# Performance work log

Hardware: AMD Instinct MI355X
Metric: run time of the kernel (lower is better)

The kernel has to match this reference:

```python
import jax, jax.numpy as jnp
import numpy as np

# lower-triangular <-> 3x3 symmetric matrix index maps (match torch_lotri2mat/mat2lotri)
LOTRI = np.array([[0, 1, 3], [1, 2, 4], [3, 4, 5]])
ROWS = np.array([0, 1, 1, 2, 2, 2])
COLS = np.array([0, 0, 1, 0, 1, 2])
NUM_NEWTON_ITERS = 6


def det3(A):
    # A: (N,3,3)
    return (A[:, 0, 0] * (A[:, 1, 1] * A[:, 2, 2] - A[:, 1, 2] * A[:, 2, 1])
            - A[:, 0, 1] * (A[:, 1, 0] * A[:, 2, 2] - A[:, 1, 2] * A[:, 2, 0])
            + A[:, 0, 2] * (A[:, 1, 0] * A[:, 2, 1] - A[:, 1, 1] * A[:, 2, 0]))


def inv3(A):
    # closed-form 3x3 inverse via adjugate; A: (N,3,3)
    c00 = A[:, 1, 1] * A[:, 2, 2] - A[:, 1, 2] * A[:, 2, 1]
    c01 = A[:, 0, 2] * A[:, 2, 1] - A[:, 0, 1] * A[:, 2, 2]
    c02 = A[:, 0, 1] * A[:, 1, 2] - A[:, 0, 2] * A[:, 1, 1]
    c10 = A[:, 1, 2] * A[:, 2, 0] - A[:, 1, 0] * A[:, 2, 2]
    c11 = A[:, 0, 0] * A[:, 2, 2] - A[:, 0, 2] * A[:, 2, 0]
    c12 = A[:, 0, 2] * A[:, 1, 0] - A[:, 0, 0] * A[:, 1, 2]
    c20 = A[:, 1, 0] * A[:, 2, 1] - A[:, 1, 1] * A[:, 2, 0]
    c21 = A[:, 0, 1] * A[:, 2, 0] - A[:, 0, 0] * A[:, 2, 1]
    c22 = A[:, 0, 0] * A[:, 1, 1] - A[:, 0, 1] * A[:, 1, 0]
    adj = jnp.stack([jnp.stack([c00, c01, c02], -1),
                     jnp.stack([c10, c11, c12], -1),
                     jnp.stack([c20, c21, c22], -1)], -2)  # (N,3,3)
    det = (A[:, 0, 0] * c00 + A[:, 0, 1] * c10 + A[:, 0, 2] * c20)
    return adj / det[:, None, None]


def trilinear_warp(img, ddf):
    # img: (B,C,H,W,D), ddf: (B,3,H,W,D) in voxel units; border padding (clamped corners)
    B, C, H, W, D = img.shape
    base = jnp.stack(jnp.meshgrid(jnp.arange(H), jnp.arange(W), jnp.arange(D),
                                  indexing='ij'), 0).astype(img.dtype)  # (3,H,W,D)
    coords = base[None] + ddf                                           # (B,3,H,W,D)
    c0 = jnp.floor(coords)
    frac = coords - c0
    c0i = c0.astype(jnp.int32)
    dims = jnp.array([H, W, D], jnp.int32).reshape(1, 3, 1, 1, 1)
    lo = jnp.clip(c0i, 0, dims - 1)
    hi = jnp.clip(c0i + 1, 0, dims - 1)
    imgf = img.reshape(B, C, H * W * D)

    def gather(xi, yi, zi):
        lin = (xi * W + yi) * D + zi                      # (B,H,W,D)
        idx = jnp.broadcast_to(lin.reshape(B, 1, -1), (B, C, H * W * D))
        return jnp.take_along_axis(imgf, idx, axis=2).reshape(B, C, H, W, D)

    fx, fy, fz = frac[:, 0, None], frac[:, 1, None], frac[:, 2, None]  # (B,1,H,W,D)
    x0, y0, z0 = lo[:, 0], lo[:, 1], lo[:, 2]
    x1, y1, z1 = hi[:, 0], hi[:, 1], hi[:, 2]
    out = jnp.zeros_like(img)
    for xi, wx in ((x0, 1.0 - fx), (x1, fx)):
        for yi, wy in ((y0, 1.0 - fy), (y1, fy)):
            for zi, wz in ((z0, 1.0 - fz), (z1, fz)):
                out = out + wx * wy * wz * gather(xi, yi, zi)
    return out


def ddf_jacobian(ddf):
    # Jacobian of the deformation phi(x)=x+ddf(x): J = I + d(ddf_i)/dx_j (central differences)
    rows = []
    for i in range(3):
        g = jnp.gradient(ddf[:, i], axis=(1, 2, 3))  # list of 3 arrays (B,H,W,D)
        rows.append(jnp.stack(g, axis=1))
    J = jnp.stack(rows, axis=1)                      # (B,3,3,H,W,D)
    eye = jnp.eye(3, dtype=ddf.dtype).reshape(1, 3, 3, 1, 1, 1)
    return J + eye


def newton_polar_det(X, n_iters):
    # Newton iteration for polar decomposition with determinant scaling
    U = X
    for _ in range(n_iters):
        zeta = jnp.abs(det3(U)) ** (-1.0 / 3.0)
        zU = zeta[:, None, None] * U
        U = 0.5 * (zU + inv3(jnp.swapaxes(zU, -1, -2)))
    return U


def setup_inputs() -> dict:
    key = jax.random.key(0)
    k1, k2 = jax.random.split(key)
    B, H, W, D = 2, 128, 128, 128
    dti = jax.random.normal(k1, (B, 6, H, W, D), dtype=jnp.float32)
    # smooth, realistic displacement field so J = I + grad(ddf) is well-conditioned
    g = jnp.stack(jnp.meshgrid(jnp.arange(H), jnp.arange(W), jnp.arange(D),
                               indexing='ij'), 0).astype(jnp.float32) / H  # (3,H,W,D)
    two_pi = 2.0 * jnp.pi
    amp = 2.0
    ddf = amp * jnp.stack([jnp.sin(two_pi * (g[0] + 0.5 * g[1])),
                           jnp.cos(two_pi * (g[1] + 0.5 * g[2])),
                           jnp.sin(two_pi * (g[2] + 0.5 * g[0]))], 0)  # (3,H,W,D)
    ddf = jnp.broadcast_to(ddf[None], (B, 3, H, W, D))
    ddf = ddf + 0.02 * jax.random.normal(k2, (B, 3, H, W, D), dtype=jnp.float32)
    return {"dti": dti, "ddf": ddf}


def reference(dti, ddf):
    B, _, H, W, D = dti.shape
    # 1) warp the lower-triangular DTI with trilinear interpolation (border padding)
    warped_lotri = trilinear_warp(dti, ddf)              # (B,6,H,W,D)
    # 2) lotri -> 3x3 symmetric matrices, absorb spatial dims
    Dmat = warped_lotri[:, LOTRI]                        # (B,3,3,H,W,D)
    Dns = Dmat.transpose(0, 3, 4, 5, 1, 2).reshape(-1, 3, 3)
    # 3) Jacobian of DDF, absorb spatial dims
    J = ddf_jacobian(ddf)                                # (B,3,3,H,W,D)
    Jns = J.transpose(0, 3, 4, 5, 1, 2).reshape(-1, 3, 3)
    # 4) rotation from polar decomposition (Newton, det scaling)
    R = newton_polar_det(Jns, NUM_NEWTON_ITERS)          # (N,3,3)
    # 5) finite-strain reorientation: R^T D R per voxel
    out_ns = jnp.einsum('nji,njk,nkl->nil', R, Dns, R)
    # 6) expand spatial dims, mat -> lotri
    out_mat = out_ns.reshape(B, H, W, D, 3, 3).transpose(0, 4, 5, 1, 2, 3)
    return out_mat[:, ROWS, COLS]                        # (B,6,H,W,D)
```

## Files before the change

### kernel.cpp

```cpp
#include <hip/hip_runtime.h>

#define NH 128
#define NW 128
#define ND 128
#define HWD (NH * NW * ND)
#define NWD (NW * ND)
#define NB 2

__global__ __launch_bounds__(256) void warp_dti_kernel(
    const float* __restrict__ dti,
    const float* __restrict__ ddf,
    float* __restrict__ out)
{
    const int blk   = blockIdx.x;
    const int b     = blk >> 13;
    const int blkin = blk & 8191;
    const int tid   = threadIdx.x;
    const int sp    = (blkin << 8) | tid;
    const int d     = tid & (ND - 1);
    const int w     = ((blkin & 63) << 1) | (tid >> 7);
    const int h     = blkin >> 6;

    const int dbase = b * 3 * HWD;

    const int oh_m = (h > 0)      ? -NWD : 0;
    const int oh_p = (h < NH - 1) ?  NWD : 0;
    const int ow_m = (w > 0)      ? -ND  : 0;
    const int ow_p = (w < NW - 1) ?  ND  : 0;
    const int od_m = (d > 0)      ? -1   : 0;
    const int od_p = (d < ND - 1) ?  1   : 0;

    float uc[3], hm[3], hp[3], wm[3], wp[3], dm[3], dp[3];
#pragma unroll
    for (int c = 0; c < 3; ++c) {
        const float* p = ddf + dbase + c * HWD;
        uc[c] = p[sp];
    }
#pragma unroll
    for (int c = 0; c < 3; ++c) {
        const float* p = ddf + dbase + c * HWD;
        hm[c] = p[sp + oh_m];  hp[c] = p[sp + oh_p];
        wm[c] = p[sp + ow_m];  wp[c] = p[sp + ow_p];
        dm[c] = p[sp + od_m];  dp[c] = p[sp + od_p];
    }

    const float cx = (float)h + uc[0];
    const float cy = (float)w + uc[1];
    const float cz = (float)d + uc[2];
    const float flx = floorf(cx), fly = floorf(cy), flz = floorf(cz);
    const float fx = cx - flx, fy = cy - fly, fz = cz - flz;
    const int x0 = (int)flx, y0 = (int)fly, z0 = (int)flz;
    const int xa = min(max(x0,     0), NH - 1), xb = min(max(x0 + 1, 0), NH - 1);
    const int ya = min(max(y0,     0), NW - 1), yb = min(max(y0 + 1, 0), NW - 1);
    const int za = min(max(z0,     0), ND - 1), zb = min(max(z0 + 1, 0), ND - 1);

    const int raa = (xa * NW + ya) * ND;
    const int rab = (xa * NW + yb) * ND;
    const int rba = (xb * NW + ya) * ND;
    const int rbb = (xb * NW + yb) * ND;

    int lin[8];
    lin[0] = raa + za; lin[1] = raa + zb;
    lin[2] = rab + za; lin[3] = rab + zb;
    lin[4] = rba + za; lin[5] = rba + zb;
    lin[6] = rbb + za; lin[7] = rbb + zb;

    const int ibase = b * 6 * HWD;
    float g[8][6];
#pragma unroll
    for (int c = 0; c < 8; ++c)
#pragma unroll
        for (int ch = 0; ch < 6; ++ch)
            g[c][ch] = dti[ibase + ch * HWD + lin[c]];

    __builtin_amdgcn_sched_barrier(0);

    const float sh = (oh_m == 0 || oh_p == 0) ? 1.0f : 0.5f;
    const float sw = (ow_m == 0 || ow_p == 0) ? 1.0f : 0.5f;
    const float sd = (od_m == 0 || od_p == 0) ? 1.0f : 0.5f;

    float U[3][3];
#pragma unroll
    for (int c = 0; c < 3; ++c) {
        U[c][0] = sh * (hp[c] - hm[c]);
        U[c][1] = sw * (wp[c] - wm[c]);
        U[c][2] = sd * (dp[c] - dm[c]);
    }
    U[0][0] += 1.0f; U[1][1] += 1.0f; U[2][2] += 1.0f;

#pragma unroll
    for (int it = 0; it < 6; ++it) {
        float c00 = U[1][1]*U[2][2] - U[1][2]*U[2][1];
        float c01 = U[0][2]*U[2][1] - U[0][1]*U[2][2];
        float c02 = U[0][1]*U[1][2] - U[0][2]*U[1][1];
        float c10 = U[1][2]*U[2][0] - U[1][0]*U[2][2];
        float c11 = U[0][0]*U[2][2] - U[0][2]*U[2][0];
        float c12 = U[0][2]*U[1][0] - U[0][0]*U[1][2];
        float c20 = U[1][0]*U[2][1] - U[1][1]*U[2][0];
        float c21 = U[0][1]*U[2][0] - U[0][0]*U[2][1];
        float c22 = U[0][0]*U[1][1] - U[0][1]*U[1][0];
        float det = U[0][0]*c00 + U[0][1]*c10 + U[0][2]*c20;

        float l    = __log2f(fabsf(det));
        float zeta = __builtin_amdgcn_exp2f(-0.33333333333333333f * l);
        float s    = copysignf(zeta * zeta, det);
        float hz = 0.5f * zeta;
        float hs = 0.5f * s;

        float n00 = hz*U[0][0] + c00*hs;
        float n01 = hz*U[0][1] + c10*hs;
        float n02 = hz*U[0][2] + c20*hs;
        float n10 = hz*U[1][0] + c01*hs;
        float n11 = hz*U[1][1] + c11*hs;
        float n12 = hz*U[1][2] + c21*hs;
        float n20 = hz*U[2][0] + c02*hs;
        float n21 = hz*U[2][1] + c12*hs;
        float n22 = hz*U[2][2] + c22*hs;
        U[0][0]=n00; U[0][1]=n01; U[0][2]=n02;
        U[1][0]=n10; U[1][1]=n11; U[1][2]=n12;
        U[2][0]=n20; U[2][1]=n21; U[2][2]=n22;
    }

    const float wxa = 1.0f - fx, wya = 1.0f - fy, wza = 1.0f - fz;
    float wc[8];
    wc[0] = (wxa * wya) * wza;  wc[1] = (wxa * wya) * fz;
    wc[2] = (wxa * fy)  * wza;  wc[3] = (wxa * fy)  * fz;
    wc[4] = (fx  * wya) * wza;  wc[5] = (fx  * wya) * fz;
    wc[6] = (fx  * fy)  * wza;  wc[7] = (fx  * fy)  * fz;

    float acc[6] = {0.f, 0.f, 0.f, 0.f, 0.f, 0.f};
#pragma unroll
    for (int c = 0; c < 8; ++c)
#pragma unroll
        for (int ch = 0; ch < 6; ++ch)
            acc[ch] = fmaf(wc[c], g[c][ch], acc[ch]);

    float Dm[3][3];
    Dm[0][0] = acc[0]; Dm[0][1] = acc[1]; Dm[0][2] = acc[3];
    Dm[1][0] = acc[1]; Dm[1][1] = acc[2]; Dm[1][2] = acc[4];
    Dm[2][0] = acc[3]; Dm[2][1] = acc[4]; Dm[2][2] = acc[5];

    float M[3][3];
#pragma unroll
    for (int i = 0; i < 3; ++i)
#pragma unroll
        for (int k = 0; k < 3; ++k)
            M[i][k] = U[0][i]*Dm[0][k] + U[1][i]*Dm[1][k] + U[2][i]*Dm[2][k];

    float T00 = M[0][0]*U[0][0] + M[0][1]*U[1][0] + M[0][2]*U[2][0];
    float T10 = M[1][0]*U[0][0] + M[1][1]*U[1][0] + M[1][2]*U[2][0];
    float T11 = M[1][0]*U[0][1] + M[1][1]*U[1][1] + M[1][2]*U[2][1];
    float T20 = M[2][0]*U[0][0] + M[2][1]*U[1][0] + M[2][2]*U[2][0];
    float T21 = M[2][0]*U[0][1] + M[2][1]*U[1][1] + M[2][2]*U[2][1];
    float T22 = M[2][0]*U[0][2] + M[2][1]*U[1][2] + M[2][2]*U[2][2];

    const int obase = b * 6 * HWD;
    out[obase + 0 * HWD + sp] = T00;
    out[obase + 1 * HWD + sp] = T10;
    out[obase + 2 * HWD + sp] = T11;
    out[obase + 3 * HWD + sp] = T20;
    out[obase + 4 * HWD + sp] = T21;
    out[obase + 5 * HWD + sp] = T22;
}

extern "C" void kernel_launch(void* const* d_in, const int* in_sizes, int n_in,
                              void* d_out, int out_size, void* d_ws, size_t ws_size,
                              hipStream_t stream) {
    const float* dti = (const float*)d_in[0];
    const float* ddf = (const float*)d_in[1];
    float* o = (float*)d_out;
    const int n = NB * HWD;
    warp_dti_kernel<<<n / 256, 256, 0, stream>>>(dti, ddf, o);
}
```

Before: 299.3 us.

## Pair z-neighbor gathers into dwordx2 loads and overlap them with Newton iterations

The 48 scalar gathers of the trilinear warp become 24 64-bit loads, each fetching both z-neighbours. Clamping the z index to ND-2 keeps the pair in range, and the weights are remapped so border clamping still gives the same result. The loads are issued through inline asm before the Newton polar iterations, with an explicit vmcnt wait placed after them, so the gather latency overlaps the ALU work. The risks are the unaligned 8-byte accesses, the fragility of hand-written asm (raw waitcnt, sgpr base constraint), and higher register pressure from keeping loads in flight.

```diff
diff --git a/kernel.cpp b/kernel.cpp
--- a/kernel.cpp
+++ b/kernel.cpp
@@ -6,6 +6,8 @@
 #define HWD (NH * NW * ND)
 #define NWD (NW * ND)
 #define NB 2
+
+typedef float f32x2 __attribute__((ext_vector_type(2)));
 
 __global__ __launch_bounds__(256) void warp_dti_kernel(
     const float* __restrict__ dti,
@@ -35,45 +37,10 @@
     for (int c = 0; c < 3; ++c) {
         const float* p = ddf + dbase + c * HWD;
         uc[c] = p[sp];
-    }
-#pragma unroll
-    for (int c = 0; c < 3; ++c) {
-        const float* p = ddf + dbase + c * HWD;
         hm[c] = p[sp + oh_m];  hp[c] = p[sp + oh_p];
         wm[c] = p[sp + ow_m];  wp[c] = p[sp + ow_p];
         dm[c] = p[sp + od_m];  dp[c] = p[sp + od_p];
     }
-
-    const float cx = (float)h + uc[0];
-    const float cy = (float)w + uc[1];
-    const float cz = (float)d + uc[2];
-    const float flx = floorf(cx), fly = floorf(cy), flz = floorf(cz);
-    const float fx = cx - flx, fy = cy - fly, fz = cz - flz;
-    const int x0 = (int)flx, y0 = (int)fly, z0 = (int)flz;
-    const int xa = min(max(x0,     0), NH - 1), xb = min(max(x0 + 1, 0), NH - 1);
-    const int ya = min(max(y0,     0), NW - 1), yb = min(max(y0 + 1, 0), NW - 1);
-    const int za = min(max(z0,     0), ND - 1), zb = min(max(z0 + 1, 0), ND - 1);
-
-    const int raa = (xa * NW + ya) * ND;
-    const int rab = (xa * NW + yb) * ND;
-    const int rba = (xb * NW + ya) * ND;
-    const int rbb = (xb * NW + yb) * ND;
-
-    int lin[8];
-    lin[0] = raa + za; lin[1] = raa + zb;
-    lin[2] = rab + za; lin[3] = rab + zb;
-    lin[4] = rba + za; lin[5] = rba + zb;
-    lin[6] = rbb + za; lin[7] = rbb + zb;
-
-    const int ibase = b * 6 * HWD;
-    float g[8][6];
-#pragma unroll
-    for (int c = 0; c < 8; ++c)
-#pragma unroll
-        for (int ch = 0; ch < 6; ++ch)
-            g[c][ch] = dti[ibase + ch * HWD + lin[c]];
-
-    __builtin_amdgcn_sched_barrier(0);
 
     const float sh = (oh_m == 0 || oh_p == 0) ? 1.0f : 0.5f;
     const float sw = (ow_m == 0 || ow_p == 0) ? 1.0f : 0.5f;
@@ -87,6 +54,37 @@
         U[c][2] = sd * (dp[c] - dm[c]);
     }
     U[0][0] += 1.0f; U[1][1] += 1.0f; U[2][2] += 1.0f;
+
+    const float cx = (float)h + uc[0];
+    const float cy = (float)w + uc[1];
+    const float cz = (float)d + uc[2];
+    const float flx = floorf(cx), fly = floorf(cy), flz = floorf(cz);
+    const float fx = cx - flx, fy = cy - fly, fz = cz - flz;
+    const int x0 = (int)flx, y0 = (int)fly, z0 = (int)flz;
+    const int xa = min(max(x0,     0), NH - 1), xb = min(max(x0 + 1, 0), NH - 1);
+    const int ya = min(max(y0,     0), NW - 1), yb = min(max(y0 + 1, 0), NW - 1);
+    const int pa = min(max(z0, 0), ND - 2);
+
+    unsigned voffs[4];
+    voffs[0] = (unsigned)(((xa * NW + ya) * ND) + pa) * 4u;
+    voffs[1] = (unsigned)(((xa * NW + yb) * ND) + pa) * 4u;
+    voffs[2] = (unsigned)(((xb * NW + ya) * ND) + pa) * 4u;
+    voffs[3] = (unsigned)(((xb * NW + yb) * ND) + pa) * 4u;
+
+    const float* bases[6];
+#pragma unroll
+    for (int ch = 0; ch < 6; ++ch)
+        bases[ch] = dti + (size_t)(b * 6 + ch) * HWD;
+
+    __builtin_amdgcn_sched_barrier(0);
+    f32x2 g[6][4];
+#pragma unroll
+    for (int ch = 0; ch < 6; ++ch)
+#pragma unroll
+        for (int c = 0; c < 4; ++c)
+            asm volatile("global_load_dwordx2 %0, %1, %2"
+                         : "=v"(g[ch][c])
+                         : "v"(voffs[c]), "s"(bases[ch]));
 
 #pragma unroll
     for (int it = 0; it < 6; ++it) {
@@ -121,19 +119,26 @@
         U[2][0]=n20; U[2][1]=n21; U[2][2]=n22;
     }
 
-    const float wxa = 1.0f - fx, wya = 1.0f - fy, wza = 1.0f - fz;
-    float wc[8];
-    wc[0] = (wxa * wya) * wza;  wc[1] = (wxa * wya) * fz;
-    wc[2] = (wxa * fy)  * wza;  wc[3] = (wxa * fy)  * fz;
-    wc[4] = (fx  * wya) * wza;  wc[5] = (fx  * wya) * fz;
-    wc[6] = (fx  * fy)  * wza;  wc[7] = (fx  * fy)  * fz;
+    const float wza = 1.0f - fz, wzb = fz;
+    const float wv0 = ((z0 <= ND - 2) ? wza : 0.0f) + ((z0 <= -1) ? wzb : 0.0f);
+    const float wv1 = ((z0 >= ND - 1) ? wza : 0.0f) + ((z0 >=  0) ? wzb : 0.0f);
+    const float wxa = 1.0f - fx, wya = 1.0f - fy;
+    float wxy[4];
+    wxy[0] = wxa * wya;  wxy[1] = wxa * fy;
+    wxy[2] = fx  * wya;  wxy[3] = fx  * fy;
+    float wA[4], wB[4];
+#pragma unroll
+    for (int c = 0; c < 4; ++c) { wA[c] = wxy[c] * wv0; wB[c] = wxy[c] * wv1; }
+
+    asm volatile("s_waitcnt vmcnt(0)" ::: "memory");
+    __builtin_amdgcn_sched_barrier(0);
 
     float acc[6] = {0.f, 0.f, 0.f, 0.f, 0.f, 0.f};
 #pragma unroll
-    for (int c = 0; c < 8; ++c)
+    for (int c = 0; c < 4; ++c)
 #pragma unroll
         for (int ch = 0; ch < 6; ++ch)
-            acc[ch] = fmaf(wc[c], g[c][ch], acc[ch]);
+            acc[ch] = fmaf(wA[c], g[ch][c].x, fmaf(wB[c], g[ch][c].y, acc[ch]));
 
     float Dm[3][3];
     Dm[0][0] = acc[0]; Dm[0][1] = acc[1]; Dm[0][2] = acc[3];
```

Result: faster. 265.5 us (-11.3%).
